# Optimization experiments

Hardware: AMD Instinct MI355X
Metric: run time of the kernel (lower is better)

The kernel has to match this reference:

```python
import jax, jax.numpy as jnp
import numpy as np

V, B, L, NG = 50000, 128, 350, 3        # vocab, batch(docs), doc length, n-gram window
D, H, C = 768, 256, 20                  # bert dim, num_hidden, class_num
HEADS, LAYERS, K, ALPHA = 8, 2, 3, 0.15 # GAT heads/layers, diffusion hops k, alpha


def setup_inputs() -> dict:
    rng = np.random.default_rng(0)
    # per-doc graphs: 350 unique word-ids per doc (nodes), n-gram window edges
    node_ids = np.stack([rng.choice(V, L, replace=False) for _ in range(B)]).ravel()
    src_b, dst_b = [], []
    for i in range(L):
        for j in range(max(0, i - NG), min(L, i + NG + 1)):
            src_b.append(i); dst_b.append(j)
    src_b, dst_b = np.asarray(src_b), np.asarray(dst_b)
    off = (np.arange(B) * L)[:, None]
    edge_src = (src_b[None, :] + off).ravel()
    edge_dst = (dst_b[None, :] + off).ravel()
    graph_id = np.repeat(np.arange(B), L)

    ks = jax.random.split(jax.random.key(0), 8)
    f32 = jnp.float32
    return {
        'node_ids': jnp.asarray(node_ids, jnp.int32),
        'edge_src': jnp.asarray(edge_src, jnp.int32),
        'edge_dst': jnp.asarray(edge_dst, jnp.int32),
        'graph_id': jnp.asarray(graph_id, jnp.int32),
        'emb':    (jax.random.normal(ks[0], (V, D), f32) * 0.02),
        'W1':     (jax.random.normal(ks[1], (D, H), f32) / np.sqrt(D)).astype(f32),
        'b1':     jnp.zeros((H,), f32),
        'W2':     (jax.random.normal(ks[2], (H, C), f32) / np.sqrt(H)).astype(f32),
        'b2':     jnp.zeros((C,), f32),
        'gat_W':  (jax.random.normal(ks[3], (LAYERS, HEADS, C, C), f32) / np.sqrt(C)).astype(f32),
        'a_src':  (jax.random.normal(ks[4], (LAYERS, HEADS, C), f32) * 0.1),
        'a_dst':  (jax.random.normal(ks[5], (LAYERS, HEADS, C), f32) * 0.1),
        'w_gate': (jax.random.normal(ks[6], (C,), f32) / np.sqrt(C)).astype(f32),
        'b_gate': jnp.zeros((), f32),
    }


def _gat_layer(h, W, a_s, a_d, src, dst, N):
    # h: [N,C]; W: [Hd,C,C]; a_s/a_d: [Hd,C]
    z = jnp.einsum('nc,hcd->hnd', h, W)                     # [Hd,N,C]
    e = jax.nn.leaky_relu(jnp.einsum('hnd,hd->hn', z, a_s)[:, src]
                          + jnp.einsum('hnd,hd->hn', z, a_d)[:, dst], 0.2)  # [Hd,E]

    def segsoftmax(ev):  # edge softmax over incoming edges at each dst node
        m = jax.ops.segment_max(ev, dst, num_segments=N)
        ex = jnp.exp(ev - m[dst])
        s = jax.ops.segment_sum(ex, dst, num_segments=N)
        return ex / (s[dst] + 1e-9)

    att = jax.vmap(segsoftmax)(e)                           # [Hd,E]

    def diffuse(zh, ah):  # attention diffusion: Z_t = (1-a) A Z_{t-1} + a Z_0
        zt = zh
        for _ in range(K):
            agg = jax.ops.segment_sum(ah[:, None] * zt[src], dst, num_segments=N)
            zt = (1.0 - ALPHA) * agg + ALPHA * zh
        return zt

    out = jax.vmap(diffuse)(z, att)                         # [Hd,N,C]
    return jax.nn.elu(out).mean(axis=0)                     # merge='mean'


def reference(node_ids, edge_src, edge_dst, graph_id, emb, W1, b1, W2, b2,
              gat_W, a_src, a_dst, w_gate, b_gate):
    N = node_ids.shape[0]
    x = emb[node_ids]                                       # [N,768] gather
    x = jax.nn.relu(x @ W1 + b1)                            # linear1 + ReLU
    h = x @ W2 + b2                                         # linear2 -> [N,C]
    for l in range(LAYERS):
        h = _gat_layer(h, gat_W[l], a_src[l], a_dst[l], edge_src, edge_dst, N)
    gate = jax.nn.sigmoid(h @ w_gate + b_gate)[:, None]     # WeightAndSum gate
    return jax.ops.segment_sum(gate * h, graph_id, num_segments=B)  # [B,C]
```

## Files before the change

### kernel.cpp

```cpp
#include <hip/hip_runtime.h>
#include <hip/hip_bf16.h>
#include <cstddef>

#define NB_NODES 44800
#define NDOCS 128
#define DLEN 350
#define DIM 768
#define HID 256
#define NCLS 20
#define NHEADS 8
#define ASTRH 264
#define ZROW 352

typedef __bf16 v8bf __attribute__((ext_vector_type(8)));
typedef __bf16 v4bf __attribute__((ext_vector_type(4)));
typedef __bf16 v2bf __attribute__((ext_vector_type(2)));
typedef float v4f __attribute__((ext_vector_type(4)));
typedef float v2f __attribute__((ext_vector_type(2)));

__global__ __launch_bounds__(256) void k_pack(const float* __restrict__ W1,
                                              __bf16* __restrict__ W1P) {
  int idx = blockIdx.x * 256 + threadIdx.x;
  int e = idx & 7;
  int l = (idx >> 3) & 63;
  int rest = idx >> 9;
  int ks = rest % 24;
  int cb = rest / 24;
  int k = ks * 32 + (l >> 4) * 8 + e;
  int col = cb * 16 + (l & 15);
  W1P[idx] = (__bf16)W1[k * 256 + col];
}

__global__ __launch_bounds__(256) void k_mlp(
    const int* __restrict__ node_ids, const float* __restrict__ emb,
    const __bf16* __restrict__ W1P, const float* __restrict__ b1,
    const float* __restrict__ W2, const float* __restrict__ b2,
    float* __restrict__ h0) {
  __shared__ __align__(16) char smem[33792];
  __bf16* As  = (__bf16*)smem;
  float*  xs  = (float*)smem;
  __bf16* w2s = (__bf16*)(smem + 16640);
  int tid = threadIdx.x;
  int wave = tid >> 6, lane = tid & 63;
  int quad = lane >> 4, l16 = lane & 15;
  int m0 = blockIdx.x * 64;

  int r0 = wave * 16;
  int nid[16];
#pragma unroll
  for (int rr = 0; rr < 16; ++rr) nid[rr] = node_ids[m0 + r0 + rr];

  v4f acc[4][4];
#pragma unroll
  for (int ms = 0; ms < 4; ++ms)
#pragma unroll
    for (int j = 0; j < 4; ++j) acc[ms][j] = (v4f){0.f, 0.f, 0.f, 0.f};

  const __bf16* wpB = W1P + (size_t)wave * 49152 + lane * 8;

#pragma unroll 1
  for (int p = 0; p < 3; ++p) {
    v4f t[16];
#pragma unroll
    for (int rr = 0; rr < 16; ++rr)
      t[rr] = *(const v4f*)(emb + (size_t)nid[rr] * DIM + p * 256 + lane * 4);
    if (p) __syncthreads();
#pragma unroll
    for (int rr = 0; rr < 16; ++rr) {
      v4bf b;
#pragma unroll
      for (int e = 0; e < 4; ++e) b[e] = (__bf16)t[rr][e];
      *(v4bf*)(As + (r0 + rr) * ASTRH + lane * 4) = b;
    }
    __syncthreads();

#pragma unroll 4
    for (int k8 = 0; k8 < 8; ++k8) {
      int ks = p * 8 + k8;
      v8bf af[4], bv[4];
#pragma unroll
      for (int ms = 0; ms < 4; ++ms)
        af[ms] = *(const v8bf*)(As + (ms * 16 + l16) * ASTRH + k8 * 32 + quad * 8);
#pragma unroll
      for (int j = 0; j < 4; ++j)
        bv[j] = *(const v8bf*)(wpB + j * 12288 + ks * 512);
#pragma unroll
      for (int ms = 0; ms < 4; ++ms)
#pragma unroll
        for (int j = 0; j < 4; ++j)
          acc[ms][j] = __builtin_amdgcn_mfma_f32_16x16x32_bf16(af[ms], bv[j], acc[ms][j], 0, 0, 0);
    }
  }

  __syncthreads();
  for (int i = tid; i < HID * NCLS; i += 256) w2s[i] = (__bf16)W2[i];

#pragma unroll
  for (int ms = 0; ms < 4; ++ms) {
    if (ms) __syncthreads();
#pragma unroll
    for (int j = 0; j < 4; ++j) {
      int col = wave * 64 + j * 16 + l16;
      float bb = b1[col];
#pragma unroll
      for (int r = 0; r < 4; ++r) {
        int lr = quad * 4 + r;
        float v = acc[ms][j][r] + bb;
        xs[lr * 260 + col] = v > 0.f ? v : 0.f;
      }
    }
    __syncthreads();
    if (tid < 160) {
      int m = tid / 10, c0 = (tid % 10) * 2;
      float s0 = b2[c0], s1 = b2[c0 + 1];
      for (int k = 0; k < HID; ++k) {
        float x = xs[m * 260 + k];
        v2bf w = *(const v2bf*)(w2s + k * NCLS + c0);
        s0 += x * (float)w[0]; s1 += x * (float)w[1];
      }
      v2f o; o[0] = s0; o[1] = s1;
      *(v2f*)(h0 + (size_t)(m0 + ms * 16 + m) * NCLS + c0) = o;
    }
  }
}

__global__ __launch_bounds__(384) void k_gat(
    const float* __restrict__ hin, const float* __restrict__ gatW,
    const float* __restrict__ a_src, const float* __restrict__ a_dst,
    int layer, float* __restrict__ zout) {
  __shared__ float zT[NCLS * ZROW];
  __shared__ float asv[DLEN], adv[DLEN];
  int tid = threadIdx.x;
  int head = blockIdx.x & 7;
  int doc = blockIdx.x >> 3;
  const float* W  = gatW  + (size_t)(layer * NHEADS + head) * NCLS * NCLS;
  const float* av = a_src + (layer * NHEADS + head) * NCLS;
  const float* dv = a_dst + (layer * NHEADS + head) * NCLS;
  int r = tid;
  bool act = r < DLEN;

  float z0[NCLS];
  if (act) {
    const float* hr = hin + ((size_t)doc * DLEN + r) * NCLS;
    float h[NCLS];
#pragma unroll
    for (int q = 0; q < 5; ++q) {
      v4f t = *(const v4f*)(hr + q * 4);
#pragma unroll
      for (int e = 0; e < 4; ++e) h[q * 4 + e] = t[e];
    }
    float zacc[NCLS];
#pragma unroll
    for (int d = 0; d < NCLS; ++d) zacc[d] = 0.f;
#pragma unroll
    for (int c = 0; c < NCLS; ++c) {
      float hc = h[c];
#pragma unroll
      for (int d = 0; d < NCLS; ++d) zacc[d] += hc * W[c * NCLS + d];
    }
    float sa = 0.f, sd = 0.f;
#pragma unroll
    for (int d = 0; d < NCLS; ++d) { sa += zacc[d] * av[d]; sd += zacc[d] * dv[d]; }
    asv[r] = sa; adv[r] = sd;
#pragma unroll
    for (int c = 0; c < NCLS; ++c) zT[c * ZROW + r] = zacc[c];
#pragma unroll
    for (int d = 0; d < NCLS; ++d) z0[d] = zacc[d];
  }
  __syncthreads();

  float att[7];
  if (act) {
    float ad = adv[r];
    float e[7]; float m = -1e30f;
#pragma unroll
    for (int j = 0; j < 7; ++j) {
      int s = r - 3 + j;
      bool valid = (s >= 0) && (s < DLEN);
      float x = valid ? asv[s] + ad : -1e30f;
      x = x > 0.f ? x : 0.2f * x;
      e[j] = valid ? x : -1e30f;
      if (e[j] > m) m = e[j];
    }
    float sum = 0.f;
#pragma unroll
    for (int j = 0; j < 7; ++j) {
      float ex = (e[j] > -1e29f) ? expf(e[j] - m) : 0.f;
      e[j] = ex; sum += ex;
    }
    float inv = 1.f / (sum + 1e-9f);
#pragma unroll
    for (int j = 0; j < 7; ++j) att[j] = e[j] * inv;
  }

  float vn[NCLS];
  for (int hop = 0; hop < 3; ++hop) {
    if (act) {
      float agg[NCLS];
#pragma unroll
      for (int c = 0; c < NCLS; ++c) agg[c] = 0.f;
#pragma unroll
      for (int j = 0; j < 7; ++j) {
        int s = r - 3 + j;
        s = s < 0 ? 0 : (s > DLEN - 1 ? DLEN - 1 : s);
        float a = att[j];
#pragma unroll
        for (int c = 0; c < NCLS; ++c) agg[c] += a * zT[c * ZROW + s];
      }
#pragma unroll
      for (int c = 0; c < NCLS; ++c) vn[c] = 0.85f * agg[c] + 0.15f * z0[c];
    }
    if (hop < 2) {
      __syncthreads();
      if (act) {
#pragma unroll
        for (int c = 0; c < NCLS; ++c) zT[c * ZROW + r] = vn[c];
      }
      __syncthreads();
    }
  }

  if (act) {
    float* og = zout + ((size_t)head * NB_NODES + (size_t)doc * DLEN + r) * NCLS;
#pragma unroll
    for (int q = 0; q < 5; ++q) {
      v4f t;
#pragma unroll
      for (int e = 0; e < 4; ++e) {
        float x = vn[q * 4 + e];
        t[e] = x > 0.f ? x : expf(x) - 1.f;
      }
      *(v4f*)(og + q * 4) = t;
    }
  }
}

__global__ __launch_bounds__(256) void k_headmean(
    const float* __restrict__ eluzt, float* __restrict__ hout) {
  int idx = blockIdx.x * 256 + threadIdx.x;
  v4f s = (v4f){0.f, 0.f, 0.f, 0.f};
#pragma unroll
  for (int h = 0; h < NHEADS; ++h)
    s += ((const v4f*)eluzt)[(size_t)h * (NB_NODES * NCLS / 4) + idx];
  v4f o; o[0] = s[0] * 0.125f; o[1] = s[1] * 0.125f; o[2] = s[2] * 0.125f; o[3] = s[3] * 0.125f;
  ((v4f*)hout)[idx] = o;
}

__global__ __launch_bounds__(384) void k_hm_pool(
    const float* __restrict__ eluzt, const float* __restrict__ w_gate,
    const float* __restrict__ b_gate, float* __restrict__ out) {
  __shared__ float red[6][NCLS];
  int tid = threadIdx.x;
  int doc = blockIdx.x;
  int r = tid;
  bool act = r < DLEN;

  float wg[NCLS];
#pragma unroll
  for (int c = 0; c < NCLS; ++c) wg[c] = w_gate[c];
  float contrib[NCLS];
#pragma unroll
  for (int c = 0; c < NCLS; ++c) contrib[c] = 0.f;
  if (act) {
    float hm[NCLS];
#pragma unroll
    for (int c = 0; c < NCLS; ++c) hm[c] = 0.f;
#pragma unroll
    for (int hd = 0; hd < NHEADS; ++hd) {
      const float* p = eluzt + ((size_t)hd * NB_NODES + (size_t)doc * DLEN + r) * NCLS;
#pragma unroll
      for (int q = 0; q < 5; ++q) {
        v4f t = *(const v4f*)(p + q * 4);
#pragma unroll
        for (int e = 0; e < 4; ++e) hm[q * 4 + e] += t[e];
      }
    }
    float d = b_gate[0];
#pragma unroll
    for (int c = 0; c < NCLS; ++c) { hm[c] *= 0.125f; d += hm[c] * wg[c]; }
    float g = 1.f / (1.f + expf(-d));
#pragma unroll
    for (int c = 0; c < NCLS; ++c) contrib[c] = g * hm[c];
  }
#pragma unroll
  for (int off = 32; off > 0; off >>= 1)
#pragma unroll
    for (int c = 0; c < NCLS; ++c) contrib[c] += __shfl_down(contrib[c], off);
  int wave = tid >> 6, lane = tid & 63;
  if (lane == 0)
#pragma unroll
    for (int c = 0; c < NCLS; ++c) red[wave][c] = contrib[c];
  __syncthreads();
  if (tid < NCLS) {
    float s = 0.f;
#pragma unroll
    for (int w = 0; w < 6; ++w) s += red[w][tid];
    out[doc * NCLS + tid] = s;
  }
}

extern "C" void kernel_launch(void* const* d_in, const int* in_sizes, int n_in,
                              void* d_out, int out_size, void* d_ws, size_t ws_size,
                              hipStream_t stream) {
  const int* node_ids = (const int*)d_in[0];
  const float* emb    = (const float*)d_in[4];
  const float* W1     = (const float*)d_in[5];
  const float* b1     = (const float*)d_in[6];
  const float* W2     = (const float*)d_in[7];
  const float* b2     = (const float*)d_in[8];
  const float* gatW   = (const float*)d_in[9];
  const float* a_src  = (const float*)d_in[10];
  const float* a_dst  = (const float*)d_in[11];
  const float* w_gate = (const float*)d_in[12];
  const float* b_gate = (const float*)d_in[13];
  float* out = (float*)d_out;
  char* ws = (char*)d_ws;

  __bf16* W1P = (__bf16*)(ws + 0);
  float* hA  = (float*)(ws + 393216);
  float* hB  = (float*)(ws + 3977216);
  float* zt  = (float*)(ws + 7561216);

  k_pack<<<768, 256, 0, stream>>>(W1, W1P);
  k_mlp<<<NB_NODES / 64, 256, 0, stream>>>(node_ids, emb, W1P, b1, W2, b2, hA);
  k_gat<<<NDOCS * NHEADS, 384, 0, stream>>>(hA, gatW, a_src, a_dst, 0, zt);
  k_headmean<<<(NB_NODES * NCLS / 4) / 256, 256, 0, stream>>>(zt, hB);
  k_gat<<<NDOCS * NHEADS, 384, 0, stream>>>(hB, gatW, a_src, a_dst, 1, zt);
  k_hm_pool<<<NDOCS, 384, 0, stream>>>(zt, w_gate, b_gate, out);
}
```

Measured before the change: 349.8 us.

## Fuse head-mean and gated pooling into GAT kernel via last-block atomic counter

Removes the separate head-mean and pooling kernels. Each doc now keeps a counter that the eight head blocks increment atomically, and the last block to finish reduces the heads for that doc: it writes the mean for layer 0, or does gate-weighted pooling for layer 1. The counters are zeroed inside the MLP kernel. This saves two launches and their tail gaps, at the cost of threadfence synchronisation and a serialized reduction tail on one block per doc.

Measured after the change: 972.3 us. 2.78x slower.

```diff
diff --git a/kernel.cpp b/kernel.cpp
--- a/kernel.cpp
+++ b/kernel.cpp
@@ -35,7 +35,7 @@
     const int* __restrict__ node_ids, const float* __restrict__ emb,
     const __bf16* __restrict__ W1P, const float* __restrict__ b1,
     const float* __restrict__ W2, const float* __restrict__ b2,
-    float* __restrict__ h0) {
+    float* __restrict__ h0, int* __restrict__ cnt) {
   __shared__ __align__(16) char smem[33792];
   __bf16* As  = (__bf16*)smem;
   float*  xs  = (float*)smem;
@@ -45,6 +45,8 @@
   int quad = lane >> 4, l16 = lane & 15;
   int m0 = blockIdx.x * 64;
 
+  if (blockIdx.x == 0 && tid < 2 * NDOCS) cnt[tid] = 0;
+
   int r0 = wave * 16;
   int nid[16];
 #pragma unroll
@@ -127,9 +129,13 @@
 __global__ __launch_bounds__(384) void k_gat(
     const float* __restrict__ hin, const float* __restrict__ gatW,
     const float* __restrict__ a_src, const float* __restrict__ a_dst,
-    int layer, float* __restrict__ zout) {
+    int layer, float* __restrict__ zout, int* __restrict__ cnt, int mode,
+    float* __restrict__ hout, const float* __restrict__ w_gate,
+    const float* __restrict__ b_gate, float* __restrict__ out) {
   __shared__ float zT[NCLS * ZROW];
   __shared__ float asv[DLEN], adv[DLEN];
+  __shared__ float red[6][NCLS];
+  __shared__ int slast;
   int tid = threadIdx.x;
   int head = blockIdx.x & 7;
   int doc = blockIdx.x >> 3;
@@ -233,69 +239,68 @@
       *(v4f*)(og + q * 4) = t;
     }
   }
-}
-
-__global__ __launch_bounds__(256) void k_headmean(
-    const float* __restrict__ eluzt, float* __restrict__ hout) {
-  int idx = blockIdx.x * 256 + threadIdx.x;
-  v4f s = (v4f){0.f, 0.f, 0.f, 0.f};
-#pragma unroll
-  for (int h = 0; h < NHEADS; ++h)
-    s += ((const v4f*)eluzt)[(size_t)h * (NB_NODES * NCLS / 4) + idx];
-  v4f o; o[0] = s[0] * 0.125f; o[1] = s[1] * 0.125f; o[2] = s[2] * 0.125f; o[3] = s[3] * 0.125f;
-  ((v4f*)hout)[idx] = o;
-}
-
-__global__ __launch_bounds__(384) void k_hm_pool(
-    const float* __restrict__ eluzt, const float* __restrict__ w_gate,
-    const float* __restrict__ b_gate, float* __restrict__ out) {
-  __shared__ float red[6][NCLS];
-  int tid = threadIdx.x;
-  int doc = blockIdx.x;
-  int r = tid;
-  bool act = r < DLEN;
-
-  float wg[NCLS];
-#pragma unroll
-  for (int c = 0; c < NCLS; ++c) wg[c] = w_gate[c];
-  float contrib[NCLS];
-#pragma unroll
-  for (int c = 0; c < NCLS; ++c) contrib[c] = 0.f;
-  if (act) {
-    float hm[NCLS];
-#pragma unroll
-    for (int c = 0; c < NCLS; ++c) hm[c] = 0.f;
-#pragma unroll
-    for (int hd = 0; hd < NHEADS; ++hd) {
-      const float* p = eluzt + ((size_t)hd * NB_NODES + (size_t)doc * DLEN + r) * NCLS;
-#pragma unroll
-      for (int q = 0; q < 5; ++q) {
-        v4f t = *(const v4f*)(p + q * 4);
-#pragma unroll
-        for (int e = 0; e < 4; ++e) hm[q * 4 + e] += t[e];
-      }
-    }
-    float d = b_gate[0];
-#pragma unroll
-    for (int c = 0; c < NCLS; ++c) { hm[c] *= 0.125f; d += hm[c] * wg[c]; }
-    float g = 1.f / (1.f + expf(-d));
-#pragma unroll
-    for (int c = 0; c < NCLS; ++c) contrib[c] = g * hm[c];
-  }
-#pragma unroll
-  for (int off = 32; off > 0; off >>= 1)
-#pragma unroll
-    for (int c = 0; c < NCLS; ++c) contrib[c] += __shfl_down(contrib[c], off);
-  int wave = tid >> 6, lane = tid & 63;
-  if (lane == 0)
-#pragma unroll
-    for (int c = 0; c < NCLS; ++c) red[wave][c] = contrib[c];
+
+  __threadfence();
   __syncthreads();
-  if (tid < NCLS) {
-    float s = 0.f;
-#pragma unroll
-    for (int w = 0; w < 6; ++w) s += red[w][tid];
-    out[doc * NCLS + tid] = s;
+  if (tid == 0) {
+    int old = atomicAdd(&cnt[doc], 1);
+    slast = (old == NHEADS - 1);
+  }
+  __syncthreads();
+  if (!slast) return;
+  __threadfence();
+
+  if (mode == 0) {
+    size_t base = (size_t)doc * DLEN * NCLS / 4;
+    for (int i = tid; i < DLEN * NCLS / 4; i += 384) {
+      v4f s = (v4f){0.f, 0.f, 0.f, 0.f};
+#pragma unroll
+      for (int hd = 0; hd < NHEADS; ++hd)
+        s += ((const v4f*)zout)[(size_t)hd * (NB_NODES * NCLS / 4) + base + i];
+      v4f o; o[0] = s[0] * 0.125f; o[1] = s[1] * 0.125f;
+      o[2] = s[2] * 0.125f; o[3] = s[3] * 0.125f;
+      ((v4f*)hout)[base + i] = o;
+    }
+  } else {
+    float contrib[NCLS];
+#pragma unroll
+    for (int c = 0; c < NCLS; ++c) contrib[c] = 0.f;
+    if (act) {
+      float hm[NCLS];
+#pragma unroll
+      for (int c = 0; c < NCLS; ++c) hm[c] = 0.f;
+#pragma unroll
+      for (int hd = 0; hd < NHEADS; ++hd) {
+        const float* p = zout + ((size_t)hd * NB_NODES + (size_t)doc * DLEN + r) * NCLS;
+#pragma unroll
+        for (int q = 0; q < 5; ++q) {
+          v4f t = *(const v4f*)(p + q * 4);
+#pragma unroll
+          for (int e = 0; e < 4; ++e) hm[q * 4 + e] += t[e];
+        }
+      }
+      float d = b_gate[0];
+#pragma unroll
+      for (int c = 0; c < NCLS; ++c) { hm[c] *= 0.125f; d += hm[c] * w_gate[c]; }
+      float g = 1.f / (1.f + expf(-d));
+#pragma unroll
+      for (int c = 0; c < NCLS; ++c) contrib[c] = g * hm[c];
+    }
+#pragma unroll
+    for (int off = 32; off > 0; off >>= 1)
+#pragma unroll
+      for (int c = 0; c < NCLS; ++c) contrib[c] += __shfl_down(contrib[c], off);
+    int wave = tid >> 6, lane = tid & 63;
+    if (lane == 0)
+#pragma unroll
+      for (int c = 0; c < NCLS; ++c) red[wave][c] = contrib[c];
+    __syncthreads();
+    if (tid < NCLS) {
+      float s = 0.f;
+#pragma unroll
+      for (int w = 0; w < 6; ++w) s += red[w][tid];
+      out[doc * NCLS + tid] = s;
+    }
   }
 }
 
@@ -320,11 +325,12 @@
   float* hA  = (float*)(ws + 393216);
   float* hB  = (float*)(ws + 3977216);
   float* zt  = (float*)(ws + 7561216);
+  int*   cnt = (int*)(ws + 36233216);
 
   k_pack<<<768, 256, 0, stream>>>(W1, W1P);
-  k_mlp<<<NB_NODES / 64, 256, 0, stream>>>(node_ids, emb, W1P, b1, W2, b2, hA);
-  k_gat<<<NDOCS * NHEADS, 384, 0, stream>>>(hA, gatW, a_src, a_dst, 0, zt);
-  k_headmean<<<(NB_NODES * NCLS / 4) / 256, 256, 0, stream>>>(zt, hB);
-  k_gat<<<NDOCS * NHEADS, 384, 0, stream>>>(hB, gatW, a_src, a_dst, 1, zt);
-  k_hm_pool<<<NDOCS, 384, 0, stream>>>(zt, w_gate, b_gate, out);
+  k_mlp<<<NB_NODES / 64, 256, 0, stream>>>(node_ids, emb, W1P, b1, W2, b2, hA, cnt);
+  k_gat<<<NDOCS * NHEADS, 384, 0, stream>>>(hA, gatW, a_src, a_dst, 0, zt,
+                                            cnt, 0, hB, w_gate, b_gate, out);
+  k_gat<<<NDOCS * NHEADS, 384, 0, stream>>>(hB, gatW, a_src, a_dst, 1, zt,
+                                            cnt + NDOCS, 1, hB, w_gate, b_gate, out);
 }
```
